# Kernel optimization log

Hardware: AMD Instinct MI355X
Metric: run time of the kernel (lower is better)

## Reference

```python
import jax, jax.numpy as jnp
import numpy as np

def setup_inputs() -> dict:
    key = jax.random.key(0)
    k1, k2 = jax.random.split(key)
    B, T_enc, T_dec, D = 8, 2048, 2048, 512
    encoder_outputs = jax.random.normal(k1, (B, T_enc, D), dtype=jnp.float32)
    decoder_outputs = jax.random.normal(k2, (B, T_dec, D), dtype=jnp.float32)
    return {"encoder_outputs": encoder_outputs, "decoder_outputs": decoder_outputs}

def reference(encoder_outputs, decoder_outputs):
    # score[b,e,t] = sum_d enc[b,e,d] * dec[b,t,d]
    score = jnp.einsum('bed,btd->bet', encoder_outputs, decoder_outputs)
    # softmax over encoder-time axis (axis=-2)
    attn = jax.nn.softmax(score, axis=1)  # [B, T_enc, T_dec]
    # context[b,t,d] = sum_e enc[b,e,d] * attn[b,e,t]  (avoids 4D broadcast)
    context = jnp.einsum('bed,bet->btd', encoder_outputs, attn)
    return jnp.concatenate([decoder_outputs, context], axis=-1)  # [B, T_dec, 2D]
```

## Files before the change

### kernel.cpp

```cpp
#include <hip/hip_runtime.h>


typedef _Float16 f16;
typedef f16 f16x8 __attribute__((ext_vector_type(8)));
typedef f16 f16x4 __attribute__((ext_vector_type(4)));
typedef float f32x4 __attribute__((ext_vector_type(4)));

#define NB 8
#define TE 2048
#define TD 2048
#define DD 512
#define TBLK 64
#define EBLK 32
#define NCH (TE / EBLK)

#define OKHI 0
#define OKT  32768
#define OS4  73728
#define OP   110592
#define OPSZ 5120
#define OAL  120832
#define OLL  121344
#define OFLG 121600
#define SMEM_BYTES 121664

__device__ __forceinline__ int swz1k(int row, int byteInRow) {
    return row * 1024 + (byteInRow ^ ((row & 7) << 4));
}

__global__ __launch_bounds__(512, 2)
void attn_fused(const float* __restrict__ enc, const float* __restrict__ dec,
                float* __restrict__ out) {
    __shared__ __align__(16) char sm[SMEM_BYTES];
    const int tid  = threadIdx.x;
    const int b    = blockIdx.x & 7;
    const int t0   = (blockIdx.x >> 3) * TBLK;
    const int lane = tid & 63;
    const int wv   = tid >> 6;
    const int li   = lane & 15;
    const int gi   = lane >> 4;
    const int et   = wv & 1;
    const int kq   = wv >> 1;
    const float L2E = 1.44269504088896f;

    const float* encB = enc + (size_t)b * TE * DD;
    const float* decB = dec + (size_t)b * TD * DD;
    float*       outB = out + (size_t)b * TD * (2 * DD);

    const int c4 = tid & 127;
    const int rb = tid >> 7;

    f32x4 st[8];
    #pragma unroll
    for (int i = 0; i < 8; ++i)
        st[i] = *(const f32x4*)(encB + (size_t)(8 * rb + i) * DD + 4 * c4);

    f16x8 qF[4][4];
    #pragma unroll
    for (int kk = 0; kk < 4; ++kk)
        #pragma unroll
        for (int tl = 0; tl < 4; ++tl) {
            const float* qp = decB + (size_t)(t0 + 16 * tl + li) * DD
                            + 128 * kq + 32 * kk + 8 * gi;
            f32x4 q0 = *(const f32x4*)qp;
            f32x4 q1 = *(const f32x4*)(qp + 4);
            f16x8 h;
            #pragma unroll
            for (int j = 0; j < 4; ++j) { h[j] = (f16)q0[j]; h[4 + j] = (f16)q1[j]; }
            qF[kk][tl] = h;
        }

    f16x4 hvB[8];
    #pragma unroll
    for (int i = 0; i < 8; ++i) {
        f16x4 h4 = {(f16)st[i][0], (f16)st[i][1], (f16)st[i][2], (f16)st[i][3]};
        hvB[i] = h4;
        *(f16x4*)(sm + OKHI + swz1k(8 * rb + i, 8 * c4)) = h4;
    }
    #pragma unroll
    for (int i = 0; i < 8; ++i)
        st[i] = *(const f32x4*)(encB + (size_t)(EBLK + 8 * rb + i) * DD + 4 * c4);
    __syncthreads();

    const int cq   = lane & 7;
    const int erq  = lane >> 3;
    const int tcol = 8 * wv + cq;
    float mrun = -1.0e30f;
    float lpart = 0.0f;

    f32x4 ctx[4][4];
    #pragma unroll
    for (int md = 0; md < 4; ++md)
        #pragma unroll
        for (int tt = 0; tt < 4; ++tt)
            ctx[md][tt] = (f32x4){0.f, 0.f, 0.f, 0.f};

    for (int ch = 0; ch < NCH; ++ch) {
        const int pb = ch & 1;
        const int qb = pb ^ 1;
        const bool doPV = (ch > 0);
        const bool more = (ch + 1 < NCH);

        f32x4 sacc[4];
        #pragma unroll
        for (int tl = 0; tl < 4; ++tl)
            sacc[tl] = (f32x4){0.f, 0.f, 0.f, 0.f};
        __builtin_amdgcn_s_setprio(1);
        #pragma unroll
        for (int kk = 0; kk < 4; ++kk) {
            int cb = 256 * kq + 64 * kk + 16 * gi;
            f16x8 aF = *(const f16x8*)(sm + OKHI + swz1k(16 * et + li, cb));
            #pragma unroll
            for (int tl = 0; tl < 4; ++tl)
                sacc[tl] = __builtin_amdgcn_mfma_f32_16x16x32_f16(aF, qF[kk][tl], sacc[tl], 0, 0, 0);
        }
        __builtin_amdgcn_s_setprio(0);
        #pragma unroll
        for (int tl = 0; tl < 4; ++tl)
            *(f32x4*)(sm + OS4 + kq * 9216 + (16 * tl + li) * 144
                      + (16 * et + 4 * gi) * 4) = sacc[tl];
        __syncthreads();

        f32x4 s4 = (f32x4){0.f, 0.f, 0.f, 0.f};
        #pragma unroll
        for (int bu = 0; bu < 4; ++bu)
            s4 += *(const f32x4*)(sm + OS4 + bu * 9216 + tcol * 144 + 16 * erq);

        bool doR = false;
        f16x8 bP[4];
        if (doPV) {
            const uint4* fp = (const uint4*)(sm + OFLG + 32 * qb);
            uint4 f0 = fp[0], f1 = fp[1];
            doR = (f0.x | f0.y | f0.z | f0.w | f1.x | f1.y | f1.z | f1.w) != 0;
            #pragma unroll
            for (int tt = 0; tt < 4; ++tt)
                bP[tt] = *(const f16x8*)(sm + OP + OPSZ * qb + (16 * tt + li) * 80 + 16 * gi);
        }
        {
            float pml = fmaxf(fmaxf(s4[0], s4[1]), fmaxf(s4[2], s4[3]));
            bool trip = pml > mrun + 8.0f;
            unsigned long long bal = __ballot(trip);
            float alpha = 1.0f;
            if (bal != 0ULL) {
                float pm = pml;
                pm = fmaxf(pm, __shfl_xor(pm, 8));
                pm = fmaxf(pm, __shfl_xor(pm, 16));
                pm = fmaxf(pm, __shfl_xor(pm, 32));
                float mnew = fmaxf(mrun, pm);
                alpha = exp2f((mrun - mnew) * L2E);
                lpart *= alpha;
                mrun = mnew;
            }
            f32x4 p4;
            #pragma unroll
            for (int j = 0; j < 4; ++j) p4[j] = exp2f((s4[j] - mrun) * L2E);
            lpart += p4[0] + p4[1] + p4[2] + p4[3];
            f16x4 pw = {(f16)p4[0], (f16)p4[1], (f16)p4[2], (f16)p4[3]};
            *(f16x4*)(sm + OP + OPSZ * pb + tcol * 80 + 8 * erq) = pw;
            if (erq == 0) *(float*)(sm + OAL + 256 * pb + 4 * tcol) = alpha;
            if (lane == 0) *(unsigned*)(sm + OFLG + 32 * pb + 4 * wv) = (bal != 0ULL) ? 1u : 0u;
        }
        if (doPV) {
            if (doR) {
                float av[4];
                #pragma unroll
                for (int tt = 0; tt < 4; ++tt)
                    av[tt] = *(const float*)(sm + OAL + 256 * qb + 4 * (16 * tt + li));
                #pragma unroll
                for (int md = 0; md < 4; ++md)
                    #pragma unroll
                    for (int tt = 0; tt < 4; ++tt)
                        #pragma unroll
                        for (int r = 0; r < 4; ++r) ctx[md][tt][r] *= av[tt];
            }
            __builtin_amdgcn_s_setprio(1);
            #pragma unroll
            for (int md = 0; md < 4; ++md) {
                int dv = 64 * wv + 16 * md + li;
                int sig = ((dv >> 3) & 3) << 4;
                f16x8 a = *(const f16x8*)(sm + OKT + dv * 80 + ((16 * gi) ^ sig));
                #pragma unroll
                for (int tt = 0; tt < 4; ++tt)
                    ctx[md][tt] = __builtin_amdgcn_mfma_f32_16x16x32_f16(a, bP[tt], ctx[md][tt], 0, 0, 0);
            }
            __builtin_amdgcn_s_setprio(0);
        }
        f16x4 hvA[8];
        if (more) {
            #pragma unroll
            for (int i = 0; i < 8; ++i) {
                f16x4 h4 = {(f16)st[i][0], (f16)st[i][1], (f16)st[i][2], (f16)st[i][3]};
                hvA[i] = h4;
                *(f16x4*)(sm + OKHI + swz1k(8 * rb + i, 8 * c4)) = h4;
            }
            if (ch + 2 < NCH) {
                const float* src = encB + (size_t)(ch + 2) * EBLK * DD;
                #pragma unroll
                for (int i = 0; i < 8; ++i)
                    st[i] = *(const f32x4*)(src + (size_t)(8 * rb + i) * DD + 4 * c4);
            }
        }
        __syncthreads();
        #pragma unroll
        for (int k = 0; k < 4; ++k) {
            int d = 4 * c4 + k;
            int sig = ((d >> 3) & 3) << 4;
            f16x8 q8 = {hvB[0][k], hvB[1][k], hvB[2][k], hvB[3][k],
                        hvB[4][k], hvB[5][k], hvB[6][k], hvB[7][k]};
            *(f16x8*)(sm + OKT + d * 80 + ((16 * rb) ^ sig)) = q8;
        }
        if (more) {
            #pragma unroll
            for (int i = 0; i < 8; ++i) hvB[i] = hvA[i];
        }
    }

    __syncthreads();

    {
        const int qb2 = (NCH - 1) & 1;
        const uint4* fp = (const uint4*)(sm + OFLG + 32 * qb2);
        uint4 f0 = fp[0], f1 = fp[1];
        bool doR = (f0.x | f0.y | f0.z | f0.w | f1.x | f1.y | f1.z | f1.w) != 0;
        f16x8 bP[4];
        #pragma unroll
        for (int tt = 0; tt < 4; ++tt)
            bP[tt] = *(const f16x8*)(sm + OP + OPSZ * qb2 + (16 * tt + li) * 80 + 16 * gi);
        if (doR) {
            float av[4];
            #pragma unroll
            for (int tt = 0; tt < 4; ++tt)
                av[tt] = *(const float*)(sm + OAL + 256 * qb2 + 4 * (16 * tt + li));
            #pragma unroll
            for (int md = 0; md < 4; ++md)
                #pragma unroll
                for (int tt = 0; tt < 4; ++tt)
                    #pragma unroll
                    for (int r = 0; r < 4; ++r) ctx[md][tt][r] *= av[tt];
        }
        #pragma unroll
        for (int md = 0; md < 4; ++md) {
            int dv = 64 * wv + 16 * md + li;
            int sig = ((dv >> 3) & 3) << 4;
            f16x8 a = *(const f16x8*)(sm + OKT + dv * 80 + ((16 * gi) ^ sig));
            #pragma unroll
            for (int tt = 0; tt < 4; ++tt)
                ctx[md][tt] = __builtin_amdgcn_mfma_f32_16x16x32_f16(a, bP[tt], ctx[md][tt], 0, 0, 0);
        }
    }

    {
        float ps = lpart;
        ps += __shfl_xor(ps, 8);
        ps += __shfl_xor(ps, 16);
        ps += __shfl_xor(ps, 32);
        if (erq == 0) *(float*)(sm + OLL + 4 * tcol) = ps;
    }
    __syncthreads();
    float inv[4];
    #pragma unroll
    for (int tt = 0; tt < 4; ++tt)
        inv[tt] = 1.0f / *(const float*)(sm + OLL + 4 * (16 * tt + li));
    #pragma unroll
    for (int md = 0; md < 4; ++md)
        #pragma unroll
        for (int tt = 0; tt < 4; ++tt) {
            int t = t0 + 16 * tt + li;
            int d = 64 * wv + 16 * md + 4 * gi;
            float4 o;
            o.x = ctx[md][tt][0] * inv[tt];
            o.y = ctx[md][tt][1] * inv[tt];
            o.z = ctx[md][tt][2] * inv[tt];
            o.w = ctx[md][tt][3] * inv[tt];
            *(float4*)(outB + (size_t)t * (2 * DD) + DD + d) = o;
        }
    #pragma unroll
    for (int it = 0; it < TBLK * (DD / 4) / 512; ++it) {
        int i = tid + it * 512;
        int t = i >> 7, cc = i & 127;
        float4 q = ((const float4*)(decB + (size_t)(t0 + t) * DD))[cc];
        ((float4*)(outB + (size_t)(t0 + t) * (2 * DD)))[cc] = q;
    }
}

extern "C" void kernel_launch(void* const* d_in, const int* in_sizes, int n_in,
                              void* d_out, int out_size, void* d_ws, size_t ws_size,
                              hipStream_t stream) {
    const float* enc = (const float*)d_in[0];
    const float* dec = (const float*)d_in[1];
    float* out = (float*)d_out;
    dim3 grid(NB * (TD / TBLK));
    dim3 block(512);
    attn_fused<<<grid, block, 0, stream>>>(enc, dec, out);
}
```

Baseline: 134.6 us.

## Halve decoder and encoder tile sizes with 4-wave blocks and 16x16x16 MFMA

Shrinks the per-block decoder tile from 64 to 32 rows and the encoder chunk from 32 to 16 rows, using 256-thread blocks of four waves. Each wave now covers a 128-wide slice of D in both the score and context GEMMs. The PV step switches to 16x16x16 MFMA with f16x4 operands, and all LDS layouts, swizzles and the per-wave score reduction are resized to match. Shared memory drops to about 50KB and the grid doubles, aiming at more resident blocks and better latency hiding. The cost is that encoder data is re-read by twice as many blocks, chunks are smaller, and the number of barriers per unit of work roughly doubles.

```diff
diff --git a/kernel.cpp b/kernel.cpp
--- a/kernel.cpp
+++ b/kernel.cpp
@@ -4,31 +4,33 @@
 typedef _Float16 f16;
 typedef f16 f16x8 __attribute__((ext_vector_type(8)));
 typedef f16 f16x4 __attribute__((ext_vector_type(4)));
+typedef f16 f16x2 __attribute__((ext_vector_type(2)));
 typedef float f32x4 __attribute__((ext_vector_type(4)));
+typedef float f32x2 __attribute__((ext_vector_type(2)));
 
 #define NB 8
 #define TE 2048
 #define TD 2048
 #define DD 512
-#define TBLK 64
-#define EBLK 32
+#define TBLK 32
+#define EBLK 16
 #define NCH (TE / EBLK)
 
 #define OKHI 0
-#define OKT  32768
-#define OS4  73728
-#define OP   110592
-#define OPSZ 5120
-#define OAL  120832
-#define OLL  121344
-#define OFLG 121600
-#define SMEM_BYTES 121664
+#define OKT  16384
+#define OS4  36864
+#define OP   47104
+#define OPSZ 1280
+#define OAL  49664
+#define OLL  49920
+#define OFLG 50048
+#define SMEM_BYTES 50080
 
 __device__ __forceinline__ int swz1k(int row, int byteInRow) {
     return row * 1024 + (byteInRow ^ ((row & 7) << 4));
 }
 
-__global__ __launch_bounds__(512, 2)
+__global__ __launch_bounds__(256, 2)
 void attn_fused(const float* __restrict__ enc, const float* __restrict__ dec,
                 float* __restrict__ out) {
     __shared__ __align__(16) char sm[SMEM_BYTES];
@@ -39,8 +41,6 @@
     const int wv   = tid >> 6;
     const int li   = lane & 15;
     const int gi   = lane >> 4;
-    const int et   = wv & 1;
-    const int kq   = wv >> 1;
     const float L2E = 1.44269504088896f;
 
     const float* encB = enc + (size_t)b * TE * DD;
@@ -55,13 +55,13 @@
     for (int i = 0; i < 8; ++i)
         st[i] = *(const f32x4*)(encB + (size_t)(8 * rb + i) * DD + 4 * c4);
 
-    f16x8 qF[4][4];
+    f16x8 qF[4][2];
     #pragma unroll
     for (int kk = 0; kk < 4; ++kk)
         #pragma unroll
-        for (int tl = 0; tl < 4; ++tl) {
+        for (int tl = 0; tl < 2; ++tl) {
             const float* qp = decB + (size_t)(t0 + 16 * tl + li) * DD
-                            + 128 * kq + 32 * kk + 8 * gi;
+                            + 128 * wv + 32 * kk + 8 * gi;
             f32x4 q0 = *(const f32x4*)qp;
             f32x4 q1 = *(const f32x4*)(qp + 4);
             f16x8 h;
@@ -88,12 +88,12 @@
     float mrun = -1.0e30f;
     float lpart = 0.0f;
 
-    f32x4 ctx[4][4];
-    #pragma unroll
-    for (int md = 0; md < 4; ++md)
-        #pragma unroll
-        for (int tt = 0; tt < 4; ++tt)
-            ctx[md][tt] = (f32x4){0.f, 0.f, 0.f, 0.f};
+    f32x4 ctx[8][2];
+    #pragma unroll
+    for (int md = 0; md < 8; ++md) {
+        ctx[md][0] = (f32x4){0.f, 0.f, 0.f, 0.f};
+        ctx[md][1] = (f32x4){0.f, 0.f, 0.f, 0.f};
+    }
 
     for (int ch = 0; ch < NCH; ++ch) {
         const int pb = ch & 1;
@@ -101,43 +101,38 @@
         const bool doPV = (ch > 0);
         const bool more = (ch + 1 < NCH);
 
-        f32x4 sacc[4];
-        #pragma unroll
-        for (int tl = 0; tl < 4; ++tl)
-            sacc[tl] = (f32x4){0.f, 0.f, 0.f, 0.f};
+        f32x4 sacc[2];
+        sacc[0] = (f32x4){0.f, 0.f, 0.f, 0.f};
+        sacc[1] = (f32x4){0.f, 0.f, 0.f, 0.f};
         __builtin_amdgcn_s_setprio(1);
         #pragma unroll
         for (int kk = 0; kk < 4; ++kk) {
-            int cb = 256 * kq + 64 * kk + 16 * gi;
-            f16x8 aF = *(const f16x8*)(sm + OKHI + swz1k(16 * et + li, cb));
-            #pragma unroll
-            for (int tl = 0; tl < 4; ++tl)
-                sacc[tl] = __builtin_amdgcn_mfma_f32_16x16x32_f16(aF, qF[kk][tl], sacc[tl], 0, 0, 0);
+            f16x8 aF = *(const f16x8*)(sm + OKHI + swz1k(li, 256 * wv + 64 * kk + 16 * gi));
+            sacc[0] = __builtin_amdgcn_mfma_f32_16x16x32_f16(aF, qF[kk][0], sacc[0], 0, 0, 0);
+            sacc[1] = __builtin_amdgcn_mfma_f32_16x16x32_f16(aF, qF[kk][1], sacc[1], 0, 0, 0);
         }
         __builtin_amdgcn_s_setprio(0);
         #pragma unroll
-        for (int tl = 0; tl < 4; ++tl)
-            *(f32x4*)(sm + OS4 + kq * 9216 + (16 * tl + li) * 144
-                      + (16 * et + 4 * gi) * 4) = sacc[tl];
+        for (int tl = 0; tl < 2; ++tl)
+            *(f32x4*)(sm + OS4 + wv * 2560 + (16 * tl + li) * 80 + 16 * gi) = sacc[tl];
         __syncthreads();
 
-        f32x4 s4 = (f32x4){0.f, 0.f, 0.f, 0.f};
+        f32x2 s2 = (f32x2){0.f, 0.f};
         #pragma unroll
         for (int bu = 0; bu < 4; ++bu)
-            s4 += *(const f32x4*)(sm + OS4 + bu * 9216 + tcol * 144 + 16 * erq);
+            s2 += *(const f32x2*)(sm + OS4 + bu * 2560 + tcol * 80 + 8 * erq);
 
         bool doR = false;
-        f16x8 bP[4];
+        f16x4 bP[2];
         if (doPV) {
-            const uint4* fp = (const uint4*)(sm + OFLG + 32 * qb);
-            uint4 f0 = fp[0], f1 = fp[1];
-            doR = (f0.x | f0.y | f0.z | f0.w | f1.x | f1.y | f1.z | f1.w) != 0;
-            #pragma unroll
-            for (int tt = 0; tt < 4; ++tt)
-                bP[tt] = *(const f16x8*)(sm + OP + OPSZ * qb + (16 * tt + li) * 80 + 16 * gi);
+            uint4 fl = *(const uint4*)(sm + OFLG + 16 * qb);
+            doR = (fl.x | fl.y | fl.z | fl.w) != 0;
+            #pragma unroll
+            for (int tt = 0; tt < 2; ++tt)
+                bP[tt] = *(const f16x4*)(sm + OP + OPSZ * qb + (16 * tt + li) * 40 + 8 * gi);
         }
         {
-            float pml = fmaxf(fmaxf(s4[0], s4[1]), fmaxf(s4[2], s4[3]));
+            float pml = fmaxf(s2[0], s2[1]);
             bool trip = pml > mrun + 8.0f;
             unsigned long long bal = __ballot(trip);
             float alpha = 1.0f;
@@ -151,37 +146,35 @@
                 lpart *= alpha;
                 mrun = mnew;
             }
-            f32x4 p4;
-            #pragma unroll
-            for (int j = 0; j < 4; ++j) p4[j] = exp2f((s4[j] - mrun) * L2E);
-            lpart += p4[0] + p4[1] + p4[2] + p4[3];
-            f16x4 pw = {(f16)p4[0], (f16)p4[1], (f16)p4[2], (f16)p4[3]};
-            *(f16x4*)(sm + OP + OPSZ * pb + tcol * 80 + 8 * erq) = pw;
-            if (erq == 0) *(float*)(sm + OAL + 256 * pb + 4 * tcol) = alpha;
-            if (lane == 0) *(unsigned*)(sm + OFLG + 32 * pb + 4 * wv) = (bal != 0ULL) ? 1u : 0u;
+            float p0 = exp2f((s2[0] - mrun) * L2E);
+            float p1 = exp2f((s2[1] - mrun) * L2E);
+            lpart += p0 + p1;
+            f16x2 pw = {(f16)p0, (f16)p1};
+            *(f16x2*)(sm + OP + OPSZ * pb + tcol * 40 + 4 * erq) = pw;
+            if (erq == 0) *(float*)(sm + OAL + 128 * pb + 4 * tcol) = alpha;
+            if (lane == 0) *(unsigned*)(sm + OFLG + 16 * pb + 4 * wv) = (bal != 0ULL) ? 1u : 0u;
         }
         if (doPV) {
             if (doR) {
-                float av[4];
-                #pragma unroll
-                for (int tt = 0; tt < 4; ++tt)
-                    av[tt] = *(const float*)(sm + OAL + 256 * qb + 4 * (16 * tt + li));
-                #pragma unroll
-                for (int md = 0; md < 4; ++md)
+                float av[2];
+                #pragma unroll
+                for (int tt = 0; tt < 2; ++tt)
+                    av[tt] = *(const float*)(sm + OAL + 128 * qb + 4 * (16 * tt + li));
+                #pragma unroll
+                for (int md = 0; md < 8; ++md)
                     #pragma unroll
-                    for (int tt = 0; tt < 4; ++tt)
+                    for (int tt = 0; tt < 2; ++tt)
                         #pragma unroll
                         for (int r = 0; r < 4; ++r) ctx[md][tt][r] *= av[tt];
             }
             __builtin_amdgcn_s_setprio(1);
             #pragma unroll
-            for (int md = 0; md < 4; ++md) {
-                int dv = 64 * wv + 16 * md + li;
-                int sig = ((dv >> 3) & 3) << 4;
-                f16x8 a = *(const f16x8*)(sm + OKT + dv * 80 + ((16 * gi) ^ sig));
-                #pragma unroll
-                for (int tt = 0; tt < 4; ++tt)
-                    ctx[md][tt] = __builtin_amdgcn_mfma_f32_16x16x32_f16(a, bP[tt], ctx[md][tt], 0, 0, 0);
+            for (int md = 0; md < 8; ++md) {
+                int dv = 128 * wv + 16 * md + li;
+                int sig = ((dv >> 2) & 1) << 4;
+                f16x4 aV = *(const f16x4*)(sm + OKT + dv * 40 + ((8 * gi) ^ sig));
+                ctx[md][0] = __builtin_amdgcn_mfma_f32_16x16x16f16(aV, bP[0], ctx[md][0], 0, 0, 0);
+                ctx[md][1] = __builtin_amdgcn_mfma_f32_16x16x16f16(aV, bP[1], ctx[md][1], 0, 0, 0);
             }
             __builtin_amdgcn_s_setprio(0);
         }
@@ -204,10 +197,10 @@
         #pragma unroll
         for (int k = 0; k < 4; ++k) {
             int d = 4 * c4 + k;
-            int sig = ((d >> 3) & 3) << 4;
+            int sig = (c4 & 1) << 4;
             f16x8 q8 = {hvB[0][k], hvB[1][k], hvB[2][k], hvB[3][k],
                         hvB[4][k], hvB[5][k], hvB[6][k], hvB[7][k]};
-            *(f16x8*)(sm + OKT + d * 80 + ((16 * rb) ^ sig)) = q8;
+            *(f16x8*)(sm + OKT + d * 40 + ((16 * rb) ^ sig)) = q8;
         }
         if (more) {
             #pragma unroll
@@ -219,33 +212,31 @@
 
     {
         const int qb2 = (NCH - 1) & 1;
-        const uint4* fp = (const uint4*)(sm + OFLG + 32 * qb2);
-        uint4 f0 = fp[0], f1 = fp[1];
-        bool doR = (f0.x | f0.y | f0.z | f0.w | f1.x | f1.y | f1.z | f1.w) != 0;
-        f16x8 bP[4];
-        #pragma unroll
-        for (int tt = 0; tt < 4; ++tt)
-            bP[tt] = *(const f16x8*)(sm + OP + OPSZ * qb2 + (16 * tt + li) * 80 + 16 * gi);
+        uint4 fl = *(const uint4*)(sm + OFLG + 16 * qb2);
+        bool doR = (fl.x | fl.y | fl.z | fl.w) != 0;
+        f16x4 bP[2];
+        #pragma unroll
+        for (int tt = 0; tt < 2; ++tt)
+            bP[tt] = *(const f16x4*)(sm + OP + OPSZ * qb2 + (16 * tt + li) * 40 + 8 * gi);
         if (doR) {
-            float av[4];
-            #pragma unroll
-            for (int tt = 0; tt < 4; ++tt)
-                av[tt] = *(const float*)(sm + OAL + 256 * qb2 + 4 * (16 * tt + li));
-            #pragma unroll
-            for (int md = 0; md < 4; ++md)
-                #pragma unroll
-                for (int tt = 0; tt < 4; ++tt)
+            float av[2];
+            #pragma unroll
+            for (int tt = 0; tt < 2; ++tt)
+                av[tt] = *(const float*)(sm + OAL + 128 * qb2 + 4 * (16 * tt + li));
+            #pragma unroll
+            for (int md = 0; md < 8; ++md)
+                #pragma unroll
+                for (int tt = 0; tt < 2; ++tt)
                     #pragma unroll
                     for (int r = 0; r < 4; ++r) ctx[md][tt][r] *= av[tt];
         }
         #pragma unroll
-        for (int md = 0; md < 4; ++md) {
-            int dv = 64 * wv + 16 * md + li;
-            int sig = ((dv >> 3) & 3) << 4;
-            f16x8 a = *(const f16x8*)(sm + OKT + dv * 80 + ((16 * gi) ^ sig));
-            #pragma unroll
-            for (int tt = 0; tt < 4; ++tt)
-                ctx[md][tt] = __builtin_amdgcn_mfma_f32_16x16x32_f16(a, bP[tt], ctx[md][tt], 0, 0, 0);
+        for (int md = 0; md < 8; ++md) {
+            int dv = 128 * wv + 16 * md + li;
+            int sig = ((dv >> 2) & 1) << 4;
+            f16x4 aV = *(const f16x4*)(sm + OKT + dv * 40 + ((8 * gi) ^ sig));
+            ctx[md][0] = __builtin_amdgcn_mfma_f32_16x16x16f16(aV, bP[0], ctx[md][0], 0, 0, 0);
+            ctx[md][1] = __builtin_amdgcn_mfma_f32_16x16x16f16(aV, bP[1], ctx[md][1], 0, 0, 0);
         }
     }
 
@@ -257,16 +248,16 @@
         if (erq == 0) *(float*)(sm + OLL + 4 * tcol) = ps;
     }
     __syncthreads();
-    float inv[4];
-    #pragma unroll
-    for (int tt = 0; tt < 4; ++tt)
+    float inv[2];
+    #pragma unroll
+    for (int tt = 0; tt < 2; ++tt)
         inv[tt] = 1.0f / *(const float*)(sm + OLL + 4 * (16 * tt + li));
     #pragma unroll
-    for (int md = 0; md < 4; ++md)
-        #pragma unroll
-        for (int tt = 0; tt < 4; ++tt) {
+    for (int md = 0; md < 8; ++md)
+        #pragma unroll
+        for (int tt = 0; tt < 2; ++tt) {
             int t = t0 + 16 * tt + li;
-            int d = 64 * wv + 16 * md + 4 * gi;
+            int d = 128 * wv + 16 * md + 4 * gi;
             float4 o;
             o.x = ctx[md][tt][0] * inv[tt];
             o.y = ctx[md][tt][1] * inv[tt];
@@ -275,8 +266,8 @@
             *(float4*)(outB + (size_t)t * (2 * DD) + DD + d) = o;
         }
     #pragma unroll
-    for (int it = 0; it < TBLK * (DD / 4) / 512; ++it) {
-        int i = tid + it * 512;
+    for (int it = 0; it < TBLK * (DD / 4) / 256; ++it) {
+        int i = tid + it * 256;
         int t = i >> 7, cc = i & 127;
         float4 q = ((const float4*)(decB + (size_t)(t0 + t) * DD))[cc];
         ((float4*)(outB + (size_t)(t0 + t) * (2 * DD)))[cc] = q;
@@ -290,6 +281,6 @@
     const float* dec = (const float*)d_in[1];
     float* out = (float*)d_out;
     dim3 grid(NB * (TD / TBLK));
-    dim3 block(512);
+    dim3 block(256);
     attn_fused<<<grid, block, 0, stream>>>(enc, dec, out);
 }
```

Result: slower. 202.6 us (+50.5%).
